# Performance work log

Hardware: AMD Instinct MI355X
Metric: run time of the kernel (lower is better)

The kernel has to match this reference:

```python
import jax, jax.numpy as jnp
import numpy as np

D, H, L, FF, EPS = 3, 3, 12, 2048, 1e-5
B, C, T = 32, 2, 64


def _ln(x, g, b):
    m = jnp.mean(x, -1, keepdims=True)
    v = jnp.mean((x - m) ** 2, -1, keepdims=True)
    return (x - m) / jnp.sqrt(v + EPS) * g + b


def _mha(xq, xkv, w, b, ow, ob):
    # xq: [Tq,B,D], xkv: [S,B,D]; w: [3D,D] packed q/k/v like torch in_proj_weight
    Tq, Bb, _ = xq.shape
    S = xkv.shape[0]
    q = xq @ w[:D].T + b[:D]
    k = xkv @ w[D:2 * D].T + b[D:2 * D]
    v = xkv @ w[2 * D:].T + b[2 * D:]
    dh = D // H  # = 1
    q = q.reshape(Tq, Bb, H, dh)
    k = k.reshape(S, Bb, H, dh)
    v = v.reshape(S, Bb, H, dh)
    scores = jnp.einsum('qbhd,kbhd->bhqk', q, k) * (1.0 / np.sqrt(dh))
    att = jax.nn.softmax(scores, axis=-1)
    o = jnp.einsum('bhqk,kbhd->qbhd', att, v).reshape(Tq, Bb, D)
    return o @ ow.T + ob


def _ffn(x, w1, b1, w2, b2):
    return jax.nn.relu(x @ w1.T + b1) @ w2.T + b2


def _encode(x, p):
    def layer(h, pl):
        aw, ab, aow, aob, g1, b1, g2, b2, f1w, f1b, f2w, f2b = pl
        h = _ln(h + _mha(h, h, aw, ab, aow, aob), g1, b1)
        h = _ln(h + _ffn(h, f1w, f1b, f2w, f2b), g2, b2)
        return h, None
    h, _ = jax.lax.scan(layer, x, p)
    return h


def _decode(tgt, mem, p):
    def layer(h, pl):
        (sw, sb, sow, sob, cw, cb, cow, cob,
         g1, b1, g2, b2, g3, b3, f1w, f1b, f2w, f2b) = pl
        h = _ln(h + _mha(h, h, sw, sb, sow, sob), g1, b1)      # self-attn (no mask, as in source)
        h = _ln(h + _mha(h, mem, cw, cb, cow, cob), g2, b2)    # cross-attn
        h = _ln(h + _ffn(h, f1w, f1b, f2w, f2b), g3, b3)
        return h, None
    h, _ = jax.lax.scan(layer, tgt, p)
    return h


def _forward(src, angle, enc_p, enc_ng, enc_nb, dec_p, dec_ng, dec_nb):
    Bb, _, Tt = src.shape
    a = jnp.broadcast_to(angle.reshape(Bb, 1, 1), (Bb, 1, Tt))
    x = jnp.transpose(jnp.concatenate([src, a], axis=1), (2, 0, 1))  # [T,B,3]
    mem = _ln(_encode(x, enc_p), enc_ng, enc_nb)  # encoder memory is loop-invariant

    def dec(o):
        return _ln(_decode(o, mem, dec_p), dec_ng, dec_nb)

    out = jnp.zeros_like(x).at[0].set(x[0])

    def step(o, t):
        pred = dec(o)
        return o.at[t].set(pred[t]), None

    out, _ = jax.lax.scan(step, out, jnp.arange(1, Tt))
    return jnp.transpose(out, (1, 2, 0))  # [B,3,T]


def setup_inputs() -> dict:
    key = jax.random.key(0)
    it = iter(jax.random.split(key, 40))
    def n(shape, s=0.05):
        return jax.random.normal(next(it), shape, dtype=jnp.float32) * s
    inp = {
        'src': jax.random.normal(next(it), (B, C, T), dtype=jnp.float32),
        'angle': jax.random.normal(next(it), (B,), dtype=jnp.float32),
        'enc_attn_w': n((L, 3 * D, D)), 'enc_attn_b': n((L, 3 * D)),
        'enc_attn_ow': n((L, D, D)), 'enc_attn_ob': n((L, D)),
        'enc_ln1_g': jnp.ones((L, D)), 'enc_ln1_b': jnp.zeros((L, D)),
        'enc_ln2_g': jnp.ones((L, D)), 'enc_ln2_b': jnp.zeros((L, D)),
        'enc_ff1_w': n((L, FF, D)), 'enc_ff1_b': n((L, FF)),
        'enc_ff2_w': n((L, D, FF)), 'enc_ff2_b': n((L, D)),
        'enc_norm_g': jnp.ones((D,)), 'enc_norm_b': jnp.zeros((D,)),
        'dec_sa_w': n((L, 3 * D, D)), 'dec_sa_b': n((L, 3 * D)),
        'dec_sa_ow': n((L, D, D)), 'dec_sa_ob': n((L, D)),
        'dec_ca_w': n((L, 3 * D, D)), 'dec_ca_b': n((L, 3 * D)),
        'dec_ca_ow': n((L, D, D)), 'dec_ca_ob': n((L, D)),
        'dec_ln1_g': jnp.ones((L, D)), 'dec_ln1_b': jnp.zeros((L, D)),
        'dec_ln2_g': jnp.ones((L, D)), 'dec_ln2_b': jnp.zeros((L, D)),
        'dec_ln3_g': jnp.ones((L, D)), 'dec_ln3_b': jnp.zeros((L, D)),
        'dec_ff1_w': n((L, FF, D)), 'dec_ff1_b': n((L, FF)),
        'dec_ff2_w': n((L, D, FF)), 'dec_ff2_b': n((L, D)),
        'dec_norm_g': jnp.ones((D,)), 'dec_norm_b': jnp.zeros((D,)),
    }
    return inp


def reference(src, angle,
              enc_attn_w, enc_attn_b, enc_attn_ow, enc_attn_ob,
              enc_ln1_g, enc_ln1_b, enc_ln2_g, enc_ln2_b,
              enc_ff1_w, enc_ff1_b, enc_ff2_w, enc_ff2_b,
              enc_norm_g, enc_norm_b,
              dec_sa_w, dec_sa_b, dec_sa_ow, dec_sa_ob,
              dec_ca_w, dec_ca_b, dec_ca_ow, dec_ca_ob,
              dec_ln1_g, dec_ln1_b, dec_ln2_g, dec_ln2_b, dec_ln3_g, dec_ln3_b,
              dec_ff1_w, dec_ff1_b, dec_ff2_w, dec_ff2_b,
              dec_norm_g, dec_norm_b):
    enc_p = (enc_attn_w, enc_attn_b, enc_attn_ow, enc_attn_ob,
             enc_ln1_g, enc_ln1_b, enc_ln2_g, enc_ln2_b,
             enc_ff1_w, enc_ff1_b, enc_ff2_w, enc_ff2_b)
    dec_p = (dec_sa_w, dec_sa_b, dec_sa_ow, dec_sa_ob,
             dec_ca_w, dec_ca_b, dec_ca_ow, dec_ca_ob,
             dec_ln1_g, dec_ln1_b, dec_ln2_g, dec_ln2_b, dec_ln3_g, dec_ln3_b,
             dec_ff1_w, dec_ff1_b, dec_ff2_w, dec_ff2_b)
    return _forward(src, angle, enc_p, enc_norm_g, enc_norm_b, dec_p, dec_norm_g, dec_norm_b)
```

## Files before the change

### kernel.cpp

```cpp
#include <hip/hip_runtime.h>

#define DEV static __device__ __forceinline__

typedef _Float16 h2 __attribute__((ext_vector_type(2)));

DEV float fdot2f(h2 a, h2 b, float c) {
#if __has_builtin(__builtin_amdgcn_fdot2)
  return __builtin_amdgcn_fdot2(a, b, c, false);
#else
  return c + (float)a.x * (float)b.x + (float)a.y * (float)b.y;
#endif
}

DEV void ln3(float& a, float& b, float& c, const float* g, const float* bt) {
  float m = (a + b + c) * (1.0f / 3.0f);
  float d0 = a - m, d1 = b - m, d2 = c - m;
  float v = (d0 * d0 + d1 * d1 + d2 * d2) * (1.0f / 3.0f);
  float rs = rsqrtf(v + 1e-5f);
  a = fmaf(d0 * rs, g[0], bt[0]);
  b = fmaf(d1 * rs, g[1], bt[1]);
  c = fmaf(d2 * rs, g[2], bt[2]);
}

DEV unsigned pkh2(float a, float b) {
  h2 v = {(_Float16)a, (_Float16)b};
  return __builtin_bit_cast(unsigned, v);
}

__global__ void __launch_bounds__(256) prepack_kernel(
    const float* ea_w, const float* ea_b, const float* ea_ow, const float* ea_ob,
    const float* el1g, const float* el1b, const float* el2g, const float* el2b,
    const float* ef1w, const float* ef1b, const float* ef2w, const float* ef2b,
    const float* eng, const float* enb,
    const float* dsw, const float* dsb, const float* dsow, const float* dsob,
    const float* dcw, const float* dcb, const float* dcow, const float* dcob,
    const float* dl1g, const float* dl1b, const float* dl2g, const float* dl2b,
    const float* dl3g, const float* dl3b,
    const float* df1w, const float* df1b, const float* df2w, const float* df2b,
    const float* dng, const float* dnb,
    float* ws) {
  const int l = blockIdx.x, tid = threadIdx.x;
  const bool enc = l < 12;
  const int li = enc ? l : l - 12;
  const float* f1w = (enc ? ef1w : df1w) + li * 2048 * 3;
  const float* f1b = (enc ? ef1b : df1b) + li * 2048;
  const float* f2w = (enc ? ef2w : df2w) + li * 3 * 2048;
  uint4* FA4 = (uint4*)ws + (size_t)l * 2048;
  uint4* FB4 = FA4 + 1024;
  for (int jp = tid; jp < 1024; jp += 256) {
    const int j0 = jp * 2, j1 = j0 + 1;
    uint4 A;
    A.x = pkh2(f1w[j0 * 3 + 0], f1w[j1 * 3 + 0]);
    A.y = pkh2(f1w[j0 * 3 + 1], f1w[j1 * 3 + 1]);
    A.z = pkh2(f1w[j0 * 3 + 2], f1w[j1 * 3 + 2]);
    A.w = pkh2(f1b[j0], f1b[j1]);
    FA4[jp] = A;
    uint4 Bv;
    Bv.x = pkh2(f2w[j0], f2w[j1]);
    Bv.y = pkh2(f2w[2048 + j0], f2w[2048 + j1]);
    Bv.z = pkh2(f2w[4096 + j0], f2w[4096 + j1]);
    Bv.w = 0u;
    FB4[jp] = Bv;
  }
  float* S = ws + 196608 + l * 128;
  if (tid == 0) {
    const float* aw = (enc ? ea_w : dsw) + li * 27;
    const float* ab = (enc ? ea_b : dsb) + li * 9;
    const float* aow = (enc ? ea_ow : dsow) + li * 9;
    const float* aob = (enc ? ea_ob : dsob) + li * 3;
    for (int i = 0; i < 27; ++i) S[i] = aw[i];
    for (int i = 0; i < 9; ++i) S[27 + i] = ab[i];
    for (int i = 0; i < 9; ++i) S[36 + i] = aow[i];
    for (int i = 0; i < 3; ++i) S[45 + i] = aob[i];
    const float* p;
    p = (enc ? el1g : dl1g) + li * 3; for (int i = 0; i < 3; ++i) S[48 + i] = p[i];
    p = (enc ? el1b : dl1b) + li * 3; for (int i = 0; i < 3; ++i) S[51 + i] = p[i];
    p = (enc ? el2g : dl2g) + li * 3; for (int i = 0; i < 3; ++i) S[54 + i] = p[i];
    p = (enc ? el2b : dl2b) + li * 3; for (int i = 0; i < 3; ++i) S[57 + i] = p[i];
    p = (enc ? ef2b : df2b) + li * 3; for (int i = 0; i < 3; ++i) S[60 + i] = p[i];
    if (!enc) {
      const float* cw = dcw + li * 27;
      for (int i = 0; i < 9; ++i) {
        S[64 + i] = cw[i];
        S[94 + i] = cw[9 + i];
        S[106 + i] = cw[18 + i];
      }
      const float* cb = dcb + li * 9;
      for (int i = 0; i < 3; ++i) {
        S[73 + i] = cb[i];
        S[103 + i] = cb[3 + i];
        S[115 + i] = cb[6 + i];
      }
      for (int i = 0; i < 9; ++i) S[76 + i] = dcow[li * 9 + i];
      for (int i = 0; i < 3; ++i) S[85 + i] = dcob[li * 3 + i];
      p = dl3g + li * 3; for (int i = 0; i < 3; ++i) S[88 + i] = p[i];
      p = dl3b + li * 3; for (int i = 0; i < 3; ++i) S[91 + i] = p[i];
    }
  }
  if (l == 0 && tid == 1) {
    float* G = ws + 196608 + 24 * 128;
    for (int i = 0; i < 3; ++i) {
      G[i] = eng[i]; G[3 + i] = enb[i];
      G[6 + i] = dng[i]; G[9 + i] = dnb[i];
    }
  }
}

template <int NR>
DEV void ffn_core(const uint4* FA,
                  const float (&X0)[4], const float (&X1)[4], const float (&X2)[4],
                  float (&acc)[4][3], int lane) {
  h2 xd0[NR], xd1[NR], xd2[NR];
#pragma unroll
  for (int i = 0; i < NR; ++i) {
    xd0[i] = h2{(_Float16)X0[i], (_Float16)X0[i]};
    xd1[i] = h2{(_Float16)X1[i], (_Float16)X1[i]};
    xd2[i] = h2{(_Float16)X2[i], (_Float16)X2[i]};
  }
#pragma unroll
  for (int i = 0; i < NR; ++i) { acc[i][0] = 0.f; acc[i][1] = 0.f; acc[i][2] = 0.f; }
  const h2 z = {(_Float16)0, (_Float16)0};
#pragma unroll 4
  for (int kk = 0; kk < 16; ++kk) {
    const int jp = lane + (kk << 6);
    uint4 a = FA[jp];
    uint4 c = FA[1024 + jp];
    h2 wa0 = __builtin_bit_cast(h2, a.x), wa1 = __builtin_bit_cast(h2, a.y);
    h2 wa2 = __builtin_bit_cast(h2, a.z), bb = __builtin_bit_cast(h2, a.w);
    h2 wc0 = __builtin_bit_cast(h2, c.x), wc1 = __builtin_bit_cast(h2, c.y);
    h2 wc2 = __builtin_bit_cast(h2, c.z);
#pragma unroll
    for (int i = 0; i < NR; ++i) {
      h2 t = wa0 * xd0[i] + wa1 * xd1[i] + wa2 * xd2[i] + bb;
      t = __builtin_elementwise_max(t, z);
      acc[i][0] = fdot2f(wc0, t, acc[i][0]);
      acc[i][1] = fdot2f(wc1, t, acc[i][1]);
      acc[i][2] = fdot2f(wc2, t, acc[i][2]);
    }
  }
#pragma unroll
  for (int m = 1; m < 64; m <<= 1) {
#pragma unroll
    for (int i = 0; i < NR; ++i) {
      acc[i][0] += __shfl_xor(acc[i][0], m, 64);
      acc[i][1] += __shfl_xor(acc[i][1], m, 64);
      acc[i][2] += __shfl_xor(acc[i][2], m, 64);
    }
  }
}

template <bool DEC>
DEV void run_layer(const float* sm, const uint4* FA, const float (*ckv)[8],
                   float4* hv, float (*hln)[5],
                   float (*p1)[25], float (*p2)[25],
                   float (*o_s)[5], const float* glob,
                   int R, int t, bool from_os, bool wpred,
                   int wave, int lane, int tid) {
  if (wave < 12) {
    const int hd = wave % 3, c = wave / 3;
    const int p0 = c * 16;
    const float l2e = 1.44269504f;
    float xq0, xq1, xq2;
    if (DEC && from_os) {
      const bool real = lane < t;
      xq0 = real ? o_s[lane][0] : 0.f;
      xq1 = real ? o_s[lane][1] : 0.f;
      xq2 = real ? o_s[lane][2] : 0.f;
    } else {
      float4 hx = hv[lane];
      xq0 = hx.x; xq1 = hx.y; xq2 = hx.z;
    }
    float q = fmaf(sm[hd * 3], xq0,
              fmaf(sm[hd * 3 + 1], xq1,
              fmaf(sm[hd * 3 + 2], xq2, sm[27 + hd]))) * l2e;
    float den = 0.f, num = 0.f;
#pragma unroll
    for (int pp = 0; pp < 16; ++pp) {
      const int p = p0 + pp;
      float x0, x1, x2, mult;
      if (DEC && from_os) {
        const bool real = p < t;
        x0 = real ? o_s[p][0] : 0.f;
        x1 = real ? o_s[p][1] : 0.f;
        x2 = real ? o_s[p][2] : 0.f;
        mult = (p == R - 1) ? (float)(64 - t) : (p < R ? 1.f : 0.f);
      } else if (DEC) {
        const int pc = min(p, R - 1);
        float4 hx = hv[pc];
        x0 = hx.x; x1 = hx.y; x2 = hx.z;
        mult = (p == R - 1) ? (t > 0 ? (float)(64 - t) : 1.f)
                            : (p < R ? 1.f : 0.f);
      } else {
        float4 hx = hv[p];
        x0 = hx.x; x1 = hx.y; x2 = hx.z;
        mult = 1.f;
      }
      float k = fmaf(sm[9 + hd * 3], x0,
                fmaf(sm[9 + hd * 3 + 1], x1,
                fmaf(sm[9 + hd * 3 + 2], x2, sm[30 + hd])));
      float v = fmaf(sm[18 + hd * 3], x0,
                fmaf(sm[18 + hd * 3 + 1], x1,
                fmaf(sm[18 + hd * 3 + 2], x2, sm[33 + hd])));
      float e = exp2f(q * k);
      if (DEC) e *= mult;
      den += e;
      num = fmaf(e, v, num);
    }
    p1[lane][2 * wave] = den;
    p1[lane][2 * wave + 1] = num;
  } else if (DEC && from_os && wave == 12) {
    const bool real = lane < t;
    float4 hx;
    hx.x = real ? o_s[lane][0] : 0.f;
    hx.y = real ? o_s[lane][1] : 0.f;
    hx.z = real ? o_s[lane][2] : 0.f;
    hx.w = 0.f;
    hv[lane] = hx;
  }
  __syncthreads();
  if (DEC) {
    if (wave < 12) {
      const int r = lane, hd = wave % 3, c = wave / 3;
      float d0 = p1[r][0] + p1[r][6] + p1[r][12] + p1[r][18];
      float n0 = p1[r][1] + p1[r][7] + p1[r][13] + p1[r][19];
      float d1 = p1[r][2] + p1[r][8] + p1[r][14] + p1[r][20];
      float n1 = p1[r][3] + p1[r][9] + p1[r][15] + p1[r][21];
      float d2 = p1[r][4] + p1[r][10] + p1[r][16] + p1[r][22];
      float n2 = p1[r][5] + p1[r][11] + p1[r][17] + p1[r][23];
      float oh0 = __fdividef(n0, d0), oh1 = __fdividef(n1, d1), oh2 = __fdividef(n2, d2);
      float4 hx = hv[r];
      float a0 = fmaf(sm[36], oh0, fmaf(sm[37], oh1, fmaf(sm[38], oh2, sm[45]))) + hx.x;
      float a1 = fmaf(sm[39], oh0, fmaf(sm[40], oh1, fmaf(sm[41], oh2, sm[46]))) + hx.y;
      float a2 = fmaf(sm[42], oh0, fmaf(sm[43], oh1, fmaf(sm[44], oh2, sm[47]))) + hx.z;
      ln3(a0, a1, a2, sm + 48, sm + 51);
      if (wave == 0 && r < R) { hln[r][0] = a0; hln[r][1] = a1; hln[r][2] = a2; }
      float q = fmaf(sm[64 + hd * 3], a0,
                fmaf(sm[64 + hd * 3 + 1], a1,
                fmaf(sm[64 + hd * 3 + 2], a2, sm[73 + hd]))) * 1.44269504f;
      const int p0 = c * 16;
      float den = 0.f, num = 0.f;
#pragma unroll
      for (int pp = 0; pp < 16; ++pp) {
        const int p = p0 + pp;
        float e = exp2f(q * ckv[p][hd]);
        den += e;
        num = fmaf(e, ckv[p][3 + hd], num);
      }
      p2[r][2 * wave] = den;
      p2[r][2 * wave + 1] = num;
    }
    __syncthreads();
  }
  {
    const int nr = (wave < R) ? (1 + (R - 1 - wave) / 16) : 0;
    if (nr > 0) {
      const float(*pp)[25] = DEC ? p2 : p1;
      const float* ow = DEC ? sm + 76 : sm + 36;
      const float* ob = DEC ? sm + 85 : sm + 45;
      const float* lg = DEC ? sm + 54 : sm + 48;
      const float* lb = DEC ? sm + 57 : sm + 51;
      float X0[4], X1[4], X2[4];
#pragma unroll
      for (int i = 0; i < 4; ++i) {
        X0[i] = 0.f; X1[i] = 0.f; X2[i] = 0.f;
        if (i < nr) {
          const int rc = wave + 16 * i;
          float d0 = pp[rc][0] + pp[rc][6] + pp[rc][12] + pp[rc][18];
          float n0 = pp[rc][1] + pp[rc][7] + pp[rc][13] + pp[rc][19];
          float d1 = pp[rc][2] + pp[rc][8] + pp[rc][14] + pp[rc][20];
          float n1 = pp[rc][3] + pp[rc][9] + pp[rc][15] + pp[rc][21];
          float d2 = pp[rc][4] + pp[rc][10] + pp[rc][16] + pp[rc][22];
          float n2 = pp[rc][5] + pp[rc][11] + pp[rc][17] + pp[rc][23];
          float oh0 = __fdividef(n0, d0), oh1 = __fdividef(n1, d1), oh2 = __fdividef(n2, d2);
          float hr0, hr1, hr2;
          if (DEC) { hr0 = hln[rc][0]; hr1 = hln[rc][1]; hr2 = hln[rc][2]; }
          else     { float4 hx = hv[rc]; hr0 = hx.x; hr1 = hx.y; hr2 = hx.z; }
          float a0 = fmaf(ow[0], oh0, fmaf(ow[1], oh1, fmaf(ow[2], oh2, ob[0]))) + hr0;
          float a1 = fmaf(ow[3], oh0, fmaf(ow[4], oh1, fmaf(ow[5], oh2, ob[1]))) + hr1;
          float a2 = fmaf(ow[6], oh0, fmaf(ow[7], oh1, fmaf(ow[8], oh2, ob[2]))) + hr2;
          ln3(a0, a1, a2, lg, lb);
          X0[i] = a0; X1[i] = a1; X2[i] = a2;
        }
      }
      float acc[4][3];
      switch (nr) {
        case 1: ffn_core<1>(FA, X0, X1, X2, acc, lane); break;
        case 2: ffn_core<2>(FA, X0, X1, X2, acc, lane); break;
        case 3: ffn_core<3>(FA, X0, X1, X2, acc, lane); break;
        default: ffn_core<4>(FA, X0, X1, X2, acc, lane); break;
      }
      if (lane == 0) {
        const float* fg = DEC ? sm + 88 : sm + 54;
        const float* fb = DEC ? sm + 91 : sm + 57;
#pragma unroll
        for (int i = 0; i < 4; ++i) {
          if (i < nr) {
            const int r = wave + 16 * i;
            float y0 = acc[i][0] + sm[60] + X0[i];
            float y1 = acc[i][1] + sm[61] + X1[i];
            float y2 = acc[i][2] + sm[62] + X2[i];
            ln3(y0, y1, y2, fg, fb);
            float4 hx; hx.x = y0; hx.y = y1; hx.z = y2; hx.w = 0.f;
            hv[r] = hx;
            if (DEC && wpred && r == R - 1) {
              ln3(y0, y1, y2, glob + 6, glob + 9);
              o_s[t][0] = y0; o_s[t][1] = y1; o_s[t][2] = y2;
            }
          }
        }
      }
    }
    __syncthreads();
  }
}

__global__ void __launch_bounds__(1024) tf_kernel(const float* src, const float* angle,
                                                  const float* ws, float* out) {
  __shared__ float small_s[24][128];
  __shared__ float glob[16];
  __shared__ __align__(16) float4 hv[64];
  __shared__ float hln[64][5];
  __shared__ float p1[64][25];
  __shared__ float p2[64][25];
  __shared__ float o_s[64][5];
  __shared__ float ckcv[12][64][8];
  const int b = blockIdx.x;
  const int tid = threadIdx.x, wave = tid >> 6, lane = tid & 63;
  const uint4* FABg = (const uint4*)ws;
  const float* SM = ws + 196608;
  const float* GB = SM + 24 * 128;
  for (int i = tid; i < 24 * 128; i += 1024) ((float*)small_s)[i] = SM[i];
  if (tid < 16) glob[tid] = GB[tid];
  if (tid < 64) {
    float x0 = src[b * 128 + tid];
    float x1 = src[b * 128 + 64 + tid];
    float x2 = angle[b];
    float4 hx; hx.x = x0; hx.y = x1; hx.z = x2; hx.w = 0.f;
    hv[tid] = hx;
    o_s[tid][0] = (tid == 0) ? x0 : 0.f;
    o_s[tid][1] = (tid == 0) ? x1 : 0.f;
    o_s[tid][2] = (tid == 0) ? x2 : 0.f;
  }
  __syncthreads();
  for (int l = 0; l < 12; ++l)
    run_layer<false>(small_s[l], FABg + (size_t)l * 2048, nullptr,
                     hv, hln, p1, p2, o_s, glob,
                     64, 0, false, false, wave, lane, tid);
  if (tid < 64) {
    float4 hx = hv[tid];
    float a = hx.x, bb = hx.y, c = hx.z;
    ln3(a, bb, c, glob + 0, glob + 3);
    hx.x = a; hx.y = bb; hx.z = c;
    hv[tid] = hx;
  }
  __syncthreads();
  if (wave < 12) {
    const float* sm = small_s[12 + wave];
    float4 hx = hv[lane];
    float m0 = hx.x, m1 = hx.y, m2 = hx.z;
    float k0 = fmaf(sm[94], m0, fmaf(sm[95], m1, fmaf(sm[96], m2, sm[103])));
    float k1 = fmaf(sm[97], m0, fmaf(sm[98], m1, fmaf(sm[99], m2, sm[104])));
    float k2 = fmaf(sm[100], m0, fmaf(sm[101], m1, fmaf(sm[102], m2, sm[105])));
    float v0 = fmaf(sm[106], m0, fmaf(sm[107], m1, fmaf(sm[108], m2, sm[115])));
    float v1 = fmaf(sm[109], m0, fmaf(sm[110], m1, fmaf(sm[111], m2, sm[116])));
    float v2 = fmaf(sm[112], m0, fmaf(sm[113], m1, fmaf(sm[114], m2, sm[117])));
    ckcv[wave][lane][0] = k0; ckcv[wave][lane][1] = k1; ckcv[wave][lane][2] = k2;
    ckcv[wave][lane][3] = v0; ckcv[wave][lane][4] = v1; ckcv[wave][lane][5] = v2;
  }
  __syncthreads();
  for (int t = 1; t < 64; ++t) {
    const int R = t + 1;
    for (int li = 0; li < 12; ++li)
      run_layer<true>(small_s[12 + li], FABg + (size_t)(12 + li) * 2048,
                      (const float(*)[8])ckcv[li],
                      hv, hln, p1, p2, o_s, glob, R, t,
                      li == 0, li == 11, wave, lane, tid);
  }
  if (tid < 192) {
    int d = tid / 64, tt = tid % 64;
    out[b * 192 + tid] = o_s[tt][d];
  }
}

extern "C" void kernel_launch(void* const* d_in, const int* in_sizes, int n_in,
                              void* d_out, int out_size, void* d_ws, size_t ws_size,
                              hipStream_t stream) {
  (void)in_sizes; (void)n_in; (void)out_size; (void)ws_size;
  float* ws = (float*)d_ws;
  prepack_kernel<<<24, 256, 0, stream>>>(
      (const float*)d_in[2], (const float*)d_in[3], (const float*)d_in[4], (const float*)d_in[5],
      (const float*)d_in[6], (const float*)d_in[7], (const float*)d_in[8], (const float*)d_in[9],
      (const float*)d_in[10], (const float*)d_in[11], (const float*)d_in[12], (const float*)d_in[13],
      (const float*)d_in[14], (const float*)d_in[15],
      (const float*)d_in[16], (const float*)d_in[17], (const float*)d_in[18], (const float*)d_in[19],
      (const float*)d_in[20], (const float*)d_in[21], (const float*)d_in[22], (const float*)d_in[23],
      (const float*)d_in[24], (const float*)d_in[25], (const float*)d_in[26], (const float*)d_in[27],
      (const float*)d_in[28], (const float*)d_in[29],
      (const float*)d_in[30], (const float*)d_in[31], (const float*)d_in[32], (const float*)d_in[33],
      (const float*)d_in[34], (const float*)d_in[35],
      ws);
  tf_kernel<<<32, 1024, 0, stream>>>((const float*)d_in[0], (const float*)d_in[1], ws,
                                     (float*)d_out);
}
```

Measured before the change: 7.634 ms.

## Precompute per-row Q/K/V once and compute post-attention LN once per row

Measured after the change: 6.810 ms. 1.12x faster.

```diff
diff --git a/kernel.cpp b/kernel.cpp
--- a/kernel.cpp
+++ b/kernel.cpp
@@ -150,90 +150,86 @@
 }
 
 template <bool DEC>
-DEV void run_layer(const float* sm, const uint4* FA, const float (*ckv)[8],
-                   float4* hv, float (*hln)[5],
-                   float (*p1)[25], float (*p2)[25],
-                   float (*o_s)[5], const float* glob,
+DEV void run_layer(const float* sm, const uint4* FA, const float2* ckv2,
+                   float4* h4, float4* hln4, float4* xs4,
+                   float (*kq)[5], float2 (*kv2)[64],
+                   float2 (*p1t)[64], float2 (*p2t)[64],
+                   float4* o_s4, const float* glob,
                    int R, int t, bool from_os, bool wpred,
                    int wave, int lane, int tid) {
+  {
+    const int r = tid >> 4, o = tid & 15;
+    if (o < 6) {
+      float x0, x1, x2;
+      if (DEC && from_os) {
+        float4 xv = o_s4[r];
+        const bool real = r < t;
+        x0 = real ? xv.x : 0.f; x1 = real ? xv.y : 0.f; x2 = real ? xv.z : 0.f;
+      } else {
+        float4 xv = h4[r];
+        x0 = xv.x; x1 = xv.y; x2 = xv.z;
+        if (DEC && r >= R) { x0 = 0.f; x1 = 0.f; x2 = 0.f; }
+      }
+      if (o < 3) {
+        kq[r][o] = fmaf(sm[o * 3], x0,
+                   fmaf(sm[o * 3 + 1], x1, fmaf(sm[o * 3 + 2], x2, sm[27 + o])));
+      } else {
+        const int hd = o - 3;
+        float k = fmaf(sm[9 + hd * 3], x0,
+                  fmaf(sm[9 + hd * 3 + 1], x1, fmaf(sm[9 + hd * 3 + 2], x2, sm[30 + hd])));
+        float v = fmaf(sm[18 + hd * 3], x0,
+                  fmaf(sm[18 + hd * 3 + 1], x1, fmaf(sm[18 + hd * 3 + 2], x2, sm[33 + hd])));
+        kv2[hd][r] = float2{k, v};
+      }
+    } else if (o == 6 && DEC && from_os) {
+      float4 xv = o_s4[r];
+      const bool real = r < t;
+      float4 hx;
+      hx.x = real ? xv.x : 0.f; hx.y = real ? xv.y : 0.f;
+      hx.z = real ? xv.z : 0.f; hx.w = 0.f;
+      h4[r] = hx;
+    }
+  }
+  __syncthreads();
   if (wave < 12) {
     const int hd = wave % 3, c = wave / 3;
     const int p0 = c * 16;
-    const float l2e = 1.44269504f;
-    float xq0, xq1, xq2;
-    if (DEC && from_os) {
-      const bool real = lane < t;
-      xq0 = real ? o_s[lane][0] : 0.f;
-      xq1 = real ? o_s[lane][1] : 0.f;
-      xq2 = real ? o_s[lane][2] : 0.f;
-    } else {
-      float4 hx = hv[lane];
-      xq0 = hx.x; xq1 = hx.y; xq2 = hx.z;
-    }
-    float q = fmaf(sm[hd * 3], xq0,
-              fmaf(sm[hd * 3 + 1], xq1,
-              fmaf(sm[hd * 3 + 2], xq2, sm[27 + hd]))) * l2e;
+    const float q = kq[lane][hd] * 1.44269504f;
     float den = 0.f, num = 0.f;
 #pragma unroll
     for (int pp = 0; pp < 16; ++pp) {
       const int p = p0 + pp;
-      float x0, x1, x2, mult;
-      if (DEC && from_os) {
-        const bool real = p < t;
-        x0 = real ? o_s[p][0] : 0.f;
-        x1 = real ? o_s[p][1] : 0.f;
-        x2 = real ? o_s[p][2] : 0.f;
-        mult = (p == R - 1) ? (float)(64 - t) : (p < R ? 1.f : 0.f);
-      } else if (DEC) {
-        const int pc = min(p, R - 1);
-        float4 hx = hv[pc];
-        x0 = hx.x; x1 = hx.y; x2 = hx.z;
-        mult = (p == R - 1) ? (t > 0 ? (float)(64 - t) : 1.f)
-                            : (p < R ? 1.f : 0.f);
-      } else {
-        float4 hx = hv[p];
-        x0 = hx.x; x1 = hx.y; x2 = hx.z;
-        mult = 1.f;
-      }
-      float k = fmaf(sm[9 + hd * 3], x0,
-                fmaf(sm[9 + hd * 3 + 1], x1,
-                fmaf(sm[9 + hd * 3 + 2], x2, sm[30 + hd])));
-      float v = fmaf(sm[18 + hd * 3], x0,
-                fmaf(sm[18 + hd * 3 + 1], x1,
-                fmaf(sm[18 + hd * 3 + 2], x2, sm[33 + hd])));
-      float e = exp2f(q * k);
-      if (DEC) e *= mult;
+      float2 kv = kv2[hd][p];
+      float e = exp2f(q * kv.x);
+      if (DEC) {
+        e = (p > t) ? 0.f : e;
+        e = (p == t) ? e * (float)(64 - t) : e;
+      }
       den += e;
-      num = fmaf(e, v, num);
-    }
-    p1[lane][2 * wave] = den;
-    p1[lane][2 * wave + 1] = num;
-  } else if (DEC && from_os && wave == 12) {
-    const bool real = lane < t;
-    float4 hx;
-    hx.x = real ? o_s[lane][0] : 0.f;
-    hx.y = real ? o_s[lane][1] : 0.f;
-    hx.z = real ? o_s[lane][2] : 0.f;
-    hx.w = 0.f;
-    hv[lane] = hx;
+      num = fmaf(e, kv.y, num);
+    }
+    p1t[wave][lane] = float2{den, num};
   }
   __syncthreads();
   if (DEC) {
     if (wave < 12) {
-      const int r = lane, hd = wave % 3, c = wave / 3;
-      float d0 = p1[r][0] + p1[r][6] + p1[r][12] + p1[r][18];
-      float n0 = p1[r][1] + p1[r][7] + p1[r][13] + p1[r][19];
-      float d1 = p1[r][2] + p1[r][8] + p1[r][14] + p1[r][20];
-      float n1 = p1[r][3] + p1[r][9] + p1[r][15] + p1[r][21];
-      float d2 = p1[r][4] + p1[r][10] + p1[r][16] + p1[r][22];
-      float n2 = p1[r][5] + p1[r][11] + p1[r][17] + p1[r][23];
+      const int hd = wave % 3, c = wave / 3;
+      float2 P[12];
+#pragma unroll
+      for (int w2 = 0; w2 < 12; ++w2) P[w2] = p1t[w2][lane];
+      float d0 = P[0].x + P[3].x + P[6].x + P[9].x;
+      float n0 = P[0].y + P[3].y + P[6].y + P[9].y;
+      float d1 = P[1].x + P[4].x + P[7].x + P[10].x;
+      float n1 = P[1].y + P[4].y + P[7].y + P[10].y;
+      float d2 = P[2].x + P[5].x + P[8].x + P[11].x;
+      float n2 = P[2].y + P[5].y + P[8].y + P[11].y;
       float oh0 = __fdividef(n0, d0), oh1 = __fdividef(n1, d1), oh2 = __fdividef(n2, d2);
-      float4 hx = hv[r];
+      float4 hx = h4[lane];
       float a0 = fmaf(sm[36], oh0, fmaf(sm[37], oh1, fmaf(sm[38], oh2, sm[45]))) + hx.x;
       float a1 = fmaf(sm[39], oh0, fmaf(sm[40], oh1, fmaf(sm[41], oh2, sm[46]))) + hx.y;
       float a2 = fmaf(sm[42], oh0, fmaf(sm[43], oh1, fmaf(sm[44], oh2, sm[47]))) + hx.z;
       ln3(a0, a1, a2, sm + 48, sm + 51);
-      if (wave == 0 && r < R) { hln[r][0] = a0; hln[r][1] = a1; hln[r][2] = a2; }
+      if (wave == 0) hln4[lane] = float4{a0, a1, a2, 0.f};
       float q = fmaf(sm[64 + hd * 3], a0,
                 fmaf(sm[64 + hd * 3 + 1], a1,
                 fmaf(sm[64 + hd * 3 + 2], a2, sm[73 + hd]))) * 1.44269504f;
@@ -241,45 +237,49 @@
       float den = 0.f, num = 0.f;
 #pragma unroll
       for (int pp = 0; pp < 16; ++pp) {
-        const int p = p0 + pp;
-        float e = exp2f(q * ckv[p][hd]);
+        float2 kv = ckv2[hd * 64 + p0 + pp];
+        float e = exp2f(q * kv.x);
         den += e;
-        num = fmaf(e, ckv[p][3 + hd], num);
-      }
-      p2[r][2 * wave] = den;
-      p2[r][2 * wave + 1] = num;
+        num = fmaf(e, kv.y, num);
+      }
+      p2t[wave][lane] = float2{den, num};
     }
     __syncthreads();
   }
+  if (wave == 0) {
+    const float2(*pt)[64] = DEC ? p2t : p1t;
+    float2 P[12];
+#pragma unroll
+    for (int w2 = 0; w2 < 12; ++w2) P[w2] = pt[w2][lane];
+    float d0 = P[0].x + P[3].x + P[6].x + P[9].x;
+    float n0 = P[0].y + P[3].y + P[6].y + P[9].y;
+    float d1 = P[1].x + P[4].x + P[7].x + P[10].x;
+    float n1 = P[1].y + P[4].y + P[7].y + P[10].y;
+    float d2 = P[2].x + P[5].x + P[8].x + P[11].x;
+    float n2 = P[2].y + P[5].y + P[8].y + P[11].y;
+    float oh0 = __fdividef(n0, d0), oh1 = __fdividef(n1, d1), oh2 = __fdividef(n2, d2);
+    const float* ow = DEC ? sm + 76 : sm + 36;
+    const float* ob = DEC ? sm + 85 : sm + 45;
+    const float* lg = DEC ? sm + 54 : sm + 48;
+    const float* lb = DEC ? sm + 57 : sm + 51;
+    float4 rx = DEC ? hln4[lane] : h4[lane];
+    float a0 = fmaf(ow[0], oh0, fmaf(ow[1], oh1, fmaf(ow[2], oh2, ob[0]))) + rx.x;
+    float a1 = fmaf(ow[3], oh0, fmaf(ow[4], oh1, fmaf(ow[5], oh2, ob[1]))) + rx.y;
+    float a2 = fmaf(ow[6], oh0, fmaf(ow[7], oh1, fmaf(ow[8], oh2, ob[2]))) + rx.z;
+    ln3(a0, a1, a2, lg, lb);
+    xs4[lane] = float4{a0, a1, a2, 0.f};
+  }
+  __syncthreads();
   {
     const int nr = (wave < R) ? (1 + (R - 1 - wave) / 16) : 0;
     if (nr > 0) {
-      const float(*pp)[25] = DEC ? p2 : p1;
-      const float* ow = DEC ? sm + 76 : sm + 36;
-      const float* ob = DEC ? sm + 85 : sm + 45;
-      const float* lg = DEC ? sm + 54 : sm + 48;
-      const float* lb = DEC ? sm + 57 : sm + 51;
       float X0[4], X1[4], X2[4];
 #pragma unroll
       for (int i = 0; i < 4; ++i) {
         X0[i] = 0.f; X1[i] = 0.f; X2[i] = 0.f;
         if (i < nr) {
-          const int rc = wave + 16 * i;
-          float d0 = pp[rc][0] + pp[rc][6] + pp[rc][12] + pp[rc][18];
-          float n0 = pp[rc][1] + pp[rc][7] + pp[rc][13] + pp[rc][19];
-          float d1 = pp[rc][2] + pp[rc][8] + pp[rc][14] + pp[rc][20];
-          float n1 = pp[rc][3] + pp[rc][9] + pp[rc][15] + pp[rc][21];
-          float d2 = pp[rc][4] + pp[rc][10] + pp[rc][16] + pp[rc][22];
-          float n2 = pp[rc][5] + pp[rc][11] + pp[rc][17] + pp[rc][23];
-          float oh0 = __fdividef(n0, d0), oh1 = __fdividef(n1, d1), oh2 = __fdividef(n2, d2);
-          float hr0, hr1, hr2;
-          if (DEC) { hr0 = hln[rc][0]; hr1 = hln[rc][1]; hr2 = hln[rc][2]; }
-          else     { float4 hx = hv[rc]; hr0 = hx.x; hr1 = hx.y; hr2 = hx.z; }
-          float a0 = fmaf(ow[0], oh0, fmaf(ow[1], oh1, fmaf(ow[2], oh2, ob[0]))) + hr0;
-          float a1 = fmaf(ow[3], oh0, fmaf(ow[4], oh1, fmaf(ow[5], oh2, ob[1]))) + hr1;
-          float a2 = fmaf(ow[6], oh0, fmaf(ow[7], oh1, fmaf(ow[8], oh2, ob[2]))) + hr2;
-          ln3(a0, a1, a2, lg, lb);
-          X0[i] = a0; X1[i] = a1; X2[i] = a2;
+          float4 xv = xs4[wave + 16 * i];
+          X0[i] = xv.x; X1[i] = xv.y; X2[i] = xv.z;
         }
       }
       float acc[4][3];
@@ -300,11 +300,10 @@
             float y1 = acc[i][1] + sm[61] + X1[i];
             float y2 = acc[i][2] + sm[62] + X2[i];
             ln3(y0, y1, y2, fg, fb);
-            float4 hx; hx.x = y0; hx.y = y1; hx.z = y2; hx.w = 0.f;
-            hv[r] = hx;
+            h4[r] = float4{y0, y1, y2, 0.f};
             if (DEC && wpred && r == R - 1) {
               ln3(y0, y1, y2, glob + 6, glob + 9);
-              o_s[t][0] = y0; o_s[t][1] = y1; o_s[t][2] = y2;
+              o_s4[t] = float4{y0, y1, y2, 0.f};
             }
           }
         }
@@ -318,12 +317,15 @@
                                                   const float* ws, float* out) {
   __shared__ float small_s[24][128];
   __shared__ float glob[16];
-  __shared__ __align__(16) float4 hv[64];
-  __shared__ float hln[64][5];
-  __shared__ float p1[64][25];
-  __shared__ float p2[64][25];
-  __shared__ float o_s[64][5];
-  __shared__ float ckcv[12][64][8];
+  __shared__ __align__(16) float4 h4[64];
+  __shared__ __align__(16) float4 hln4[64];
+  __shared__ __align__(16) float4 xs4[64];
+  __shared__ __align__(16) float4 o_s4[64];
+  __shared__ float kq[64][5];
+  __shared__ __align__(8) float2 kv2[3][64];
+  __shared__ __align__(8) float2 p1t[12][64];
+  __shared__ __align__(8) float2 p2t[12][64];
+  __shared__ __align__(8) float2 ckcv2[12][3 * 64];
   const int b = blockIdx.x;
   const int tid = threadIdx.x, wave = tid >> 6, lane = tid & 63;
   const uint4* FABg = (const uint4*)ws;
@@ -335,50 +337,46 @@
     float x0 = src[b * 128 + tid];
     float x1 = src[b * 128 + 64 + tid];
     float x2 = angle[b];
-    float4 hx; hx.x = x0; hx.y = x1; hx.z = x2; hx.w = 0.f;
-    hv[tid] = hx;
-    o_s[tid][0] = (tid == 0) ? x0 : 0.f;
-    o_s[tid][1] = (tid == 0) ? x1 : 0.f;
-    o_s[tid][2] = (tid == 0) ? x2 : 0.f;
+    h4[tid] = float4{x0, x1, x2, 0.f};
+    o_s4[tid] = (tid == 0) ? float4{x0, x1, x2, 0.f} : float4{0.f, 0.f, 0.f, 0.f};
   }
   __syncthreads();
   for (int l = 0; l < 12; ++l)
     run_layer<false>(small_s[l], FABg + (size_t)l * 2048, nullptr,
-                     hv, hln, p1, p2, o_s, glob,
+                     h4, hln4, xs4, kq, kv2, p1t, p2t, o_s4, glob,
                      64, 0, false, false, wave, lane, tid);
   if (tid < 64) {
-    float4 hx = hv[tid];
+    float4 hx = h4[tid];
     float a = hx.x, bb = hx.y, c = hx.z;
     ln3(a, bb, c, glob + 0, glob + 3);
-    hx.x = a; hx.y = bb; hx.z = c;
-    hv[tid] = hx;
+    h4[tid] = float4{a, bb, c, 0.f};
   }
   __syncthreads();
   if (wave < 12) {
     const float* sm = small_s[12 + wave];
-    float4 hx = hv[lane];
+    float4 hx = h4[lane];
     float m0 = hx.x, m1 = hx.y, m2 = hx.z;
-    float k0 = fmaf(sm[94], m0, fmaf(sm[95], m1, fmaf(sm[96], m2, sm[103])));
-    float k1 = fmaf(sm[97], m0, fmaf(sm[98], m1, fmaf(sm[99], m2, sm[104])));
-    float k2 = fmaf(sm[100], m0, fmaf(sm[101], m1, fmaf(sm[102], m2, sm[105])));
-    float v0 = fmaf(sm[106], m0, fmaf(sm[107], m1, fmaf(sm[108], m2, sm[115])));
-    float v1 = fmaf(sm[109], m0, fmaf(sm[110], m1, fmaf(sm[111], m2, sm[116])));
-    float v2 = fmaf(sm[112], m0, fmaf(sm[113], m1, fmaf(sm[114], m2, sm[117])));
-    ckcv[wave][lane][0] = k0; ckcv[wave][lane][1] = k1; ckcv[wave][lane][2] = k2;
-    ckcv[wave][lane][3] = v0; ckcv[wave][lane][4] = v1; ckcv[wave][lane][5] = v2;
+#pragma unroll
+    for (int hd = 0; hd < 3; ++hd) {
+      float k = fmaf(sm[94 + hd * 3], m0,
+                fmaf(sm[94 + hd * 3 + 1], m1, fmaf(sm[94 + hd * 3 + 2], m2, sm[103 + hd])));
+      float v = fmaf(sm[106 + hd * 3], m0,
+                fmaf(sm[106 + hd * 3 + 1], m1, fmaf(sm[106 + hd * 3 + 2], m2, sm[115 + hd])));
+      ckcv2[wave][hd * 64 + lane] = float2{k, v};
+    }
   }
   __syncthreads();
   for (int t = 1; t < 64; ++t) {
     const int R = t + 1;
     for (int li = 0; li < 12; ++li)
       run_layer<true>(small_s[12 + li], FABg + (size_t)(12 + li) * 2048,
-                      (const float(*)[8])ckcv[li],
-                      hv, hln, p1, p2, o_s, glob, R, t,
+                      ckcv2[li],
+                      h4, hln4, xs4, kq, kv2, p1t, p2t, o_s4, glob, R, t,
                       li == 0, li == 11, wave, lane, tid);
   }
   if (tid < 192) {
     int d = tid / 64, tt = tid % 64;
-    out[b * 192 + tid] = o_s[tt][d];
+    out[b * 192 + tid] = ((const float*)o_s4)[tt * 4 + d];
   }
 }
 
```
